# Kernel optimization log

Measured on AMD Instinct MI355X. Metric: run time of the kernel, lower is better.

The kernel has to match this reference:

```python
import jax, jax.numpy as jnp
import numpy as np

D_MODEL = 768
N_HEADS = 12
HEAD = D_MODEL // N_HEADS  # 64


def setup_inputs() -> dict:
    key = jax.random.key(0)
    ks = jax.random.split(key, 9)
    s = 1.0 / np.sqrt(D_MODEL)
    x = jax.random.normal(ks[0], (2, 2048, D_MODEL), dtype=jnp.float32)
    # per-head Q/K/V projection weights stacked over heads: [H, d_model, head]
    Wq = jax.random.uniform(ks[1], (N_HEADS, D_MODEL, HEAD), minval=-s, maxval=s, dtype=jnp.float32)
    Wk = jax.random.uniform(ks[2], (N_HEADS, D_MODEL, HEAD), minval=-s, maxval=s, dtype=jnp.float32)
    Wv = jax.random.uniform(ks[3], (N_HEADS, D_MODEL, HEAD), minval=-s, maxval=s, dtype=jnp.float32)
    bq = jax.random.uniform(ks[4], (N_HEADS, HEAD), minval=-s, maxval=s, dtype=jnp.float32)
    bk = jax.random.uniform(ks[5], (N_HEADS, HEAD), minval=-s, maxval=s, dtype=jnp.float32)
    bv = jax.random.uniform(ks[6], (N_HEADS, HEAD), minval=-s, maxval=s, dtype=jnp.float32)
    Wo = jax.random.uniform(ks[7], (D_MODEL, D_MODEL), minval=-s, maxval=s, dtype=jnp.float32)
    bo = jax.random.uniform(ks[8], (D_MODEL,), minval=-s, maxval=s, dtype=jnp.float32)
    return {"x": x, "Wq": Wq, "Wk": Wk, "Wv": Wv, "bq": bq, "bk": bk, "bv": bv, "Wo": Wo, "bo": bo}


def reference(x, Wq, Wk, Wv, bq, bk, bv, Wo, bo):
    # x: [B, S, D]; weights stacked over heads [H, D, hd]
    Q = jnp.einsum('bsd,hde->bhse', x, Wq) + bq[None, :, None, :]
    K = jnp.einsum('bsd,hde->bhse', x, Wk) + bk[None, :, None, :]
    V = jnp.einsum('bsd,hde->bhse', x, Wv) + bv[None, :, None, :]
    scores = jnp.einsum('bhse,bhte->bhst', Q, K) / jnp.sqrt(jnp.float32(HEAD))
    attn = jax.nn.softmax(scores, axis=-1)  # [B, H, S, S]
    out = jnp.einsum('bhst,bhte->bhse', attn, V)  # [B, H, S, hd]
    B, H, S, E = out.shape
    out = out.transpose(0, 2, 1, 3).reshape(B, S, H * E)  # concat heads -> [B, S, D]
    return out @ Wo + bo
```

## Files before the change

### kernel.cpp

```cpp
#include <hip/hip_runtime.h>
#include <hip/hip_bf16.h>

typedef __bf16 bf16x8 __attribute__((ext_vector_type(8)));
typedef __bf16 bf16x4 __attribute__((ext_vector_type(4)));
typedef float  f32x4  __attribute__((ext_vector_type(4)));
typedef short  short4v __attribute__((ext_vector_type(4)));

#define MFMA_16x16x32(a,b,c) __builtin_amdgcn_mfma_f32_16x16x32_bf16((a),(b),(c),0,0,0)

#if __has_builtin(__builtin_amdgcn_mfma_f32_16x16x16_bf16)
__device__ inline f32x4 MFMA16(bf16x4 a, bf16x4 b, f32x4 c){
  return __builtin_amdgcn_mfma_f32_16x16x16_bf16(a, b, c, 0, 0, 0);
}
#elif __has_builtin(__builtin_amdgcn_mfma_f32_16x16x16bf16_1k)
__device__ inline f32x4 MFMA16(bf16x4 a, bf16x4 b, f32x4 c){
  return __builtin_amdgcn_mfma_f32_16x16x16bf16_1k(
      __builtin_bit_cast(short4v, a), __builtin_bit_cast(short4v, b), c, 0, 0, 0);
}
#else
__device__ inline f32x4 MFMA16(bf16x4 a, bf16x4 b, f32x4 c){
  f32x4 d;
  asm volatile("v_mfma_f32_16x16x16_bf16 %0, %1, %2, %3"
               : "=v"(d) : "v"(a), "v"(b), "v"(c));
  return d;
}
#endif

#if __has_builtin(__builtin_amdgcn_exp2f)
#define EXP2(x) __builtin_amdgcn_exp2f(x)
#else
extern "C" __device__ float __ocml_native_exp2_f32(float);
#define EXP2(x) __ocml_native_exp2_f32(x)
#endif

#if __has_builtin(__builtin_amdgcn_global_load_lds)
#define HAS_GLDS 1
__device__ inline void glds16(const __bf16* g, __bf16* l){
  __builtin_amdgcn_global_load_lds(
      (const __attribute__((address_space(1))) unsigned int*)g,
      (__attribute__((address_space(3))) unsigned int*)l, 16, 0, 0);
}
#else
#define HAS_GLDS 0
#endif

static constexpr int DM = 768;
static constexpr int NH = 12;
static constexpr int HD = 64;
static constexpr int BB = 2;
static constexpr int SS = 2048;
static constexpr int NR = BB*SS;
static constexpr int NC = 3*DM;
static constexpr int RTOT = BB*NH*SS;
static constexpr float SCALEQ = 0.125f * 1.4426950408889634f;

__device__ inline int xcd_swz(int b, int n){
  return (n % 8 == 0) ? (b % 8) * (n >> 3) + (b >> 3) : b;
}

static constexpr int PB_X = NR*DM/(4*256);
static constexpr int PB_W = 3*12*12;
static constexpr int PB_O = 12*12;
static constexpr int PB_B = (NC+255)/256;
__global__ __launch_bounds__(256) void k_prep(const float* __restrict__ x,
    const float* __restrict__ Wq, const float* __restrict__ Wk,
    const float* __restrict__ Wv, const float* __restrict__ bq,
    const float* __restrict__ bk, const float* __restrict__ bv,
    const float* __restrict__ Wo,
    __bf16* __restrict__ xb, __bf16* __restrict__ Wt,
    __bf16* __restrict__ WoT, float* __restrict__ bqkv)
{
  __shared__ float tile[64][65];
  const int blk = blockIdx.x, tid = threadIdx.x;
  if (blk < PB_X){
    int i = blk*256 + tid;
    float4 v = reinterpret_cast<const float4*>(x)[i];
    bf16x4 o; o[0]=(__bf16)v.x; o[1]=(__bf16)v.y; o[2]=(__bf16)v.z; o[3]=(__bf16)v.w;
    reinterpret_cast<bf16x4*>(xb)[i] = o;
  } else if (blk < PB_X + PB_W){
    int b2 = blk - PB_X;
    int dt = b2 % 12, h = (b2/12) % 12, m = b2/144;
    const float* W = (m==0)?Wq:((m==1)?Wk:Wv);
    float scale = (m==0)?SCALEQ:1.0f;
    int tx = tid & 63, ty = tid >> 6;
    #pragma unroll
    for (int i=0;i<16;i++){
      int dl = ty*16+i;
      tile[dl][tx] = W[(h*DM + dt*64 + dl)*HD + tx];
    }
    __syncthreads();
    #pragma unroll
    for (int i=0;i<16;i++){
      int e = ty*16+i;
      Wt[(size_t)(m*DM + h*HD + e)*DM + dt*64 + tx] = (__bf16)(tile[tx][e]*scale);
    }
  } else if (blk < PB_X + PB_W + PB_O){
    int b2 = blk - PB_X - PB_W;
    int dt = b2 % 12, ct = b2/12;
    int tx = tid & 63, ty = tid >> 6;
    #pragma unroll
    for (int i=0;i<16;i++){
      int dl = ty*16+i;
      tile[dl][tx] = Wo[(dt*64+dl)*DM + ct*64 + tx];
    }
    __syncthreads();
    #pragma unroll
    for (int i=0;i<16;i++){
      int cl = ty*16+i;
      WoT[(size_t)(ct*64+cl)*DM + dt*64 + tx] = (__bf16)tile[tx][cl];
    }
  } else {
    int c = (blk - PB_X - PB_W - PB_O)*256 + tid;
    if (c < NC){
      int m = c/DM, r = c - m*DM;
      const float* s = (m==0)?bq:((m==1)?bk:bv);
      bqkv[c] = s[r] * ((m==0)?SCALEQ:1.0f);
    }
  }
}

template<int BM, int EPI>
__global__ __launch_bounds__(256) void k_gemm(
    const __bf16* __restrict__ A, const __bf16* __restrict__ Bt,
    const float* __restrict__ bias, float* __restrict__ outF,
    __bf16* __restrict__ qb, __bf16* __restrict__ kb, __bf16* __restrict__ vb,
    int M, int N)
{
  constexpr int BN = 128, BK = 64;
  constexpr int K = DM;
  constexpr int HM = BM/2;
  constexpr int MR = BM/32;
  __shared__ __align__(16) __bf16 As[BM][BK];
  __shared__ __align__(16) __bf16 Bs[BN][BK];
  const int tid = threadIdx.x;
  const int w = tid>>6, lane = tid&63, g = lane>>4, r15 = lane&15;
  const int wr = w>>1, wc = w&1;
  const int nTM = M/BM;
  const int bx = xcd_swz(blockIdx.x, gridDim.x);
  const int mt = bx % nTM, nt = bx / nTM;
  const int m0 = mt*BM, n0 = nt*BN;

  const int rrel = lane>>3, seg = lane&7;
  const int ssrc = seg ^ rrel;

  f32x4 acc[MR][4];
  #pragma unroll
  for (int i=0;i<MR;i++)
    #pragma unroll
    for (int j=0;j<4;j++) acc[i][j] = f32x4{0.f,0.f,0.f,0.f};

  for (int k0=0;k0<K;k0+=BK){
#if HAS_GLDS
    #pragma unroll
    for (int c=0;c<BM/32;c++)
      glds16(&A[(size_t)(m0 + w*(BM/4) + c*8 + rrel)*K + k0 + ssrc*8],
             &As[w*(BM/4) + c*8][0]);
    #pragma unroll
    for (int c=0;c<4;c++)
      glds16(&Bt[(size_t)(n0 + w*32 + c*8 + rrel)*K + k0 + ssrc*8],
             &Bs[w*32 + c*8][0]);
#else
    #pragma unroll
    for (int c=0;c<BM/32;c++)
      *reinterpret_cast<uint4*>(&As[w*(BM/4) + c*8 + rrel][seg*8]) =
        *reinterpret_cast<const uint4*>(&A[(size_t)(m0 + w*(BM/4) + c*8 + rrel)*K + k0 + ssrc*8]);
    #pragma unroll
    for (int c=0;c<4;c++)
      *reinterpret_cast<uint4*>(&Bs[w*32 + c*8 + rrel][seg*8]) =
        *reinterpret_cast<const uint4*>(&Bt[(size_t)(n0 + w*32 + c*8 + rrel)*K + k0 + ssrc*8]);
#endif
    __syncthreads();
    bf16x8 af[MR][2], bfr[4][2];
    #pragma unroll
    for (int mi=0;mi<MR;mi++){
      int row = wr*HM + mi*16 + r15;
      #pragma unroll
      for (int c2=0;c2<2;c2++)
        af[mi][c2] = *reinterpret_cast<const bf16x8*>(&As[row][8*((c2*4+g) ^ (row&7))]);
    }
    #pragma unroll
    for (int ni=0;ni<4;ni++){
      int row = wc*64 + ni*16 + r15;
      #pragma unroll
      for (int c2=0;c2<2;c2++)
        bfr[ni][c2] = *reinterpret_cast<const bf16x8*>(&Bs[row][8*((c2*4+g) ^ (row&7))]);
    }
    #pragma unroll
    for (int c2=0;c2<2;c2++)
      #pragma unroll
      for (int mi=0;mi<MR;mi++)
        #pragma unroll
        for (int ni=0;ni<4;ni++)
          acc[mi][ni] = MFMA_16x16x32(af[mi][c2], bfr[ni][c2], acc[mi][ni]);
    __syncthreads();
  }

  #pragma unroll
  for (int mi=0;mi<MR;mi++){
    #pragma unroll
    for (int ni=0;ni<4;ni++){
      int row0 = m0 + wr*HM + mi*16 + 4*g;
      int col  = n0 + wc*64 + ni*16 + r15;
      float bc = bias[col];
      #pragma unroll
      for (int r=0;r<4;r++){
        float val = acc[mi][ni][r] + bc;
        int rr = row0 + r;
        if (EPI==1){
          outF[(size_t)rr*DM + col] = val;
        } else {
          int b = rr >> 11, s = rr & 2047;
          int m = col >= 2*DM ? 2 : (col >= DM ? 1 : 0);
          int c2 = col - m*DM, hh = c2>>6, ee = c2&63;
          __bf16* dst = (m==0) ? qb : ((m==1) ? kb : vb);
          dst[(((size_t)b*NH + hh)*SS + s)*HD + ee] = (__bf16)val;
        }
      }
    }
  }
}

__global__ __launch_bounds__(256) void k_vt(const __bf16* __restrict__ Vr,
                                            __bf16* __restrict__ Vt){
  __shared__ __align__(16) __bf16 tile[64][72];
  const int tid = threadIdx.x;
  const int bh = blockIdx.x >> 5, tt = blockIdx.x & 31;
  const int t0 = tt*64;
  const __bf16* src = Vr + (size_t)bh*SS*HD;
  __bf16* dst = Vt + (size_t)bh*HD*SS;
  const int rt = tid>>3, seg = tid&7;
  #pragma unroll
  for (int p=0;p<2;p++){
    int t = t0 + rt + 32*p;
    bf16x8 v = *reinterpret_cast<const bf16x8*>(&src[(size_t)t*HD + seg*8]);
    #pragma unroll
    for (int j=0;j<8;j++) tile[seg*8+j][rt+32*p - t0 + t0] = v[j];
  }
  __syncthreads();
  #pragma unroll
  for (int p=0;p<2;p++){
    int e = rt + 32*p;
    *reinterpret_cast<uint4*>(&dst[(size_t)e*SS + t0 + seg*8]) =
      *reinterpret_cast<const uint4*>(&tile[e][seg*8]);
  }
}

__global__ __launch_bounds__(256) void k_attn(
    const __bf16* __restrict__ Qb, const __bf16* __restrict__ Kb,
    const __bf16* __restrict__ Vt, float* __restrict__ oP,
    float* __restrict__ lP, __bf16* __restrict__ AO, int kvLen)
{
  constexpr int TT = 64, SK = 72;
  __shared__ __align__(16) __bf16 Ks[TT][SK];
  __shared__ __align__(16) __bf16 Vs[HD][SK];
  const int tid = threadIdx.x, w = tid>>6, lane = tid&63, g = lane>>4, r15 = lane&15;
  const int bx = xcd_swz(blockIdx.x, gridDim.x);
  const int qt = bx & 15, bh = bx >> 4;
  const int q0 = qt*128 + w*32;
  const int kv0 = blockIdx.y * kvLen;
  const __bf16* Qh = Qb + (size_t)bh*SS*HD;
  const __bf16* Kh = Kb + (size_t)bh*SS*HD;
  const __bf16* Vh = Vt + (size_t)bh*HD*SS;

  bf16x8 qf[2][2];
  #pragma unroll
  for (int sub=0; sub<2; sub++){
    int qrow = q0 + sub*16 + r15;
    qf[sub][0] = *reinterpret_cast<const bf16x8*>(&Qh[qrow*HD + g*8]);
    qf[sub][1] = *reinterpret_cast<const bf16x8*>(&Qh[qrow*HD + 32 + g*8]);
  }

  f32x4 o[2][4];
  #pragma unroll
  for (int s2=0;s2<2;s2++)
    #pragma unroll
    for (int i=0;i<4;i++) o[s2][i] = f32x4{0.f,0.f,0.f,0.f};
  f32x4 ol[2] = {f32x4{0.f,0.f,0.f,0.f}, f32x4{0.f,0.f,0.f,0.f}};
  const bf16x4 vones = {(__bf16)1.0f, (__bf16)1.0f, (__bf16)1.0f, (__bf16)1.0f};

  const int row0 = tid>>3,        seg0 = tid&7;
  const int row1 = (tid+256)>>3,  seg1 = tid&7;
  const int vcol0 = 32*(seg0>>2) + 16*(seg0&1) + 4*((seg0>>1)&1);

  {
    uint4 k0v = *reinterpret_cast<const uint4*>(&Kh[(kv0+row0)*HD + seg0*8]);
    uint4 k1v = *reinterpret_cast<const uint4*>(&Kh[(kv0+row1)*HD + seg1*8]);
    uint4 v0v = *reinterpret_cast<const uint4*>(&Vh[(size_t)row0*SS + kv0 + seg0*8]);
    uint4 v1v = *reinterpret_cast<const uint4*>(&Vh[(size_t)row1*SS + kv0 + seg1*8]);
    *reinterpret_cast<uint4*>(&Ks[row0][seg0*8]) = k0v;
    *reinterpret_cast<uint4*>(&Ks[row1][seg1*8]) = k1v;
    *reinterpret_cast<uint2*>(&Vs[row0][vcol0])     = uint2{v0v.x, v0v.y};
    *reinterpret_cast<uint2*>(&Vs[row0][vcol0 + 8]) = uint2{v0v.z, v0v.w};
    *reinterpret_cast<uint2*>(&Vs[row1][vcol0])     = uint2{v1v.x, v1v.y};
    *reinterpret_cast<uint2*>(&Vs[row1][vcol0 + 8]) = uint2{v1v.z, v1v.w};
  }
  __syncthreads();

  for (int t0 = kv0; t0 < kv0 + kvLen; t0 += TT){
    const bool hasNext = (t0 + TT) < kv0 + kvLen;
    uint4 k0v, k1v, v0v, v1v;
    if (hasNext){
      k0v = *reinterpret_cast<const uint4*>(&Kh[(t0+TT+row0)*HD + seg0*8]);
      k1v = *reinterpret_cast<const uint4*>(&Kh[(t0+TT+row1)*HD + seg1*8]);
      v0v = *reinterpret_cast<const uint4*>(&Vh[(size_t)row0*SS + t0+TT + seg0*8]);
      v1v = *reinterpret_cast<const uint4*>(&Vh[(size_t)row1*SS + t0+TT + seg1*8]);
    }

    bf16x8 kf0[4], kf1[4];
    #pragma unroll
    for (int jt=0;jt<4;jt++){
      kf0[jt] = *reinterpret_cast<const bf16x8*>(&Ks[jt*16 + r15][g*8]);
      kf1[jt] = *reinterpret_cast<const bf16x8*>(&Ks[jt*16 + r15][32 + g*8]);
    }
    bf16x8 vf[4][2];
    #pragma unroll
    for (int et=0;et<4;et++)
      #pragma unroll
      for (int p=0;p<2;p++)
        vf[et][p] = *reinterpret_cast<const bf16x8*>(&Vs[et*16 + r15][p*32 + g*8]);

    __syncthreads();

    if (hasNext){
      *reinterpret_cast<uint4*>(&Ks[row0][seg0*8]) = k0v;
      *reinterpret_cast<uint4*>(&Ks[row1][seg1*8]) = k1v;
      *reinterpret_cast<uint2*>(&Vs[row0][vcol0])     = uint2{v0v.x, v0v.y};
      *reinterpret_cast<uint2*>(&Vs[row0][vcol0 + 8]) = uint2{v0v.z, v0v.w};
      *reinterpret_cast<uint2*>(&Vs[row1][vcol0])     = uint2{v1v.x, v1v.y};
      *reinterpret_cast<uint2*>(&Vs[row1][vcol0 + 8]) = uint2{v1v.z, v1v.w};
    }

    f32x4 sc[2][4];
    __builtin_amdgcn_s_setprio(1);
    #pragma unroll
    for (int sub=0; sub<2; sub++)
      #pragma unroll
      for (int jt=0;jt<4;jt++){
        f32x4 t = f32x4{0.f,0.f,0.f,0.f};
        t = MFMA_16x16x32(kf0[jt], qf[sub][0], t);
        t = MFMA_16x16x32(kf1[jt], qf[sub][1], t);
        sc[sub][jt] = t;
      }
    __builtin_amdgcn_s_setprio(0);

    bf16x4 pa[2][4];
    #pragma unroll
    for (int sub=0; sub<2; sub++)
      #pragma unroll
      for (int ks=0;ks<4;ks++){
        pa[sub][ks][0] = (__bf16)EXP2(sc[sub][ks][0]);
        pa[sub][ks][1] = (__bf16)EXP2(sc[sub][ks][1]);
        pa[sub][ks][2] = (__bf16)EXP2(sc[sub][ks][2]);
        pa[sub][ks][3] = (__bf16)EXP2(sc[sub][ks][3]);
      }

    __builtin_amdgcn_s_setprio(1);
    #pragma unroll
    for (int sub=0; sub<2; sub++){
      #pragma unroll
      for (int et=0;et<4;et++)
        #pragma unroll
        for (int ks=0;ks<4;ks++){
          bf16x8 vv = vf[et][ks>>1];
          bf16x4 vq = (ks & 1) ? bf16x4{vv[4],vv[5],vv[6],vv[7]}
                               : bf16x4{vv[0],vv[1],vv[2],vv[3]};
          o[sub][et] = MFMA16(pa[sub][ks], vq, o[sub][et]);
        }
      #pragma unroll
      for (int ks=0;ks<4;ks++)
        ol[sub] = MFMA16(pa[sub][ks], vones, ol[sub]);
    }
    __builtin_amdgcn_s_setprio(0);

    __syncthreads();
  }

  const bool direct = (gridDim.y == 1);
  const int b = bh/NH, h = bh - b*NH;
  const size_t pbase = (size_t)blockIdx.y * RTOT + bh*SS;
  #pragma unroll
  for (int sub=0; sub<2; sub++){
    if (direct){
      #pragma unroll
      for (int r=0;r<4;r++){
        float linv = 1.0f / ol[sub][r];
        int s = q0 + sub*16 + 4*g + r;
        #pragma unroll
        for (int et=0;et<4;et++)
          AO[((size_t)(b*SS + s))*DM + h*HD + et*16 + r15] = (__bf16)(o[sub][et][r]*linv);
      }
    } else {
      if (r15 == 0){
        #pragma unroll
        for (int r=0;r<4;r++)
          lP[pbase + q0 + sub*16 + 4*g + r] = ol[sub][r];
      }
      #pragma unroll
      for (int r=0;r<4;r++){
        size_t rid = pbase + q0 + sub*16 + 4*g + r;
        #pragma unroll
        for (int et=0;et<4;et++)
          oP[rid*HD + et*16 + r15] = o[sub][et][r];
      }
    }
  }
}

__global__ __launch_bounds__(256) void k_merge(
    const float* __restrict__ oP, const float* __restrict__ lP,
    __bf16* __restrict__ AO, int nsplit)
{
  int t = blockIdx.x*256 + threadIdx.x;
  int rid = t >> 4, e0 = (t & 15)*4;
  int bh = rid >> 11, s = rid & 2047;
  int b = bh/NH, h = bh - b*NH;

  float lsum = 0.f;
  float acc[4] = {0.f,0.f,0.f,0.f};
  for (int sp=0; sp<nsplit; sp++){
    lsum += lP[(size_t)sp*RTOT + rid];
    float4 v = *reinterpret_cast<const float4*>(&oP[((size_t)sp*RTOT + rid)*HD + e0]);
    acc[0] += v.x; acc[1] += v.y; acc[2] += v.z; acc[3] += v.w;
  }
  float inv = 1.0f/lsum;
  size_t base = ((size_t)(b*SS + s))*DM + h*HD + e0;
  #pragma unroll
  for (int j=0;j<4;j++) AO[base + j] = (__bf16)(acc[j]*inv);
}

extern "C" void kernel_launch(void* const* d_in, const int* in_sizes, int n_in,
                              void* d_out, int out_size, void* d_ws, size_t ws_size,
                              hipStream_t stream) {
  const float* x  = (const float*)d_in[0];
  const float* Wq = (const float*)d_in[1];
  const float* Wk = (const float*)d_in[2];
  const float* Wv = (const float*)d_in[3];
  const float* bq = (const float*)d_in[4];
  const float* bk = (const float*)d_in[5];
  const float* bv = (const float*)d_in[6];
  const float* Wo = (const float*)d_in[7];
  const float* bo = (const float*)d_in[8];
  float* out = (float*)d_out;

  char* ws = (char*)d_ws;
  size_t off = 0;
  auto alloc = [&](size_t bytes) -> void* {
    void* p = ws + off;
    off += (bytes + 255) & ~size_t(255);
    return p;
  };
  __bf16* xb   = (__bf16*)alloc((size_t)NR*DM*2);
  __bf16* wt   = (__bf16*)alloc((size_t)NC*DM*2);
  float*  bqkv = (float*) alloc((size_t)NC*4);
  __bf16* wot  = (__bf16*)alloc((size_t)DM*DM*2);
  __bf16* qb2  = (__bf16*)alloc((size_t)BB*NH*SS*HD*2);
  __bf16* kb2  = (__bf16*)alloc((size_t)BB*NH*SS*HD*2);
  __bf16* vb2  = (__bf16*)alloc((size_t)BB*NH*SS*HD*2);
  __bf16* vt2  = (__bf16*)alloc((size_t)BB*NH*SS*HD*2);
  __bf16* aob  = (__bf16*)alloc((size_t)NR*DM*2);
  float*  lP   = (float*) alloc((size_t)2*RTOT*4);
  size_t  oP_off = off;
  float*  oP   = (float*)(ws + oP_off);
  auto fits = [&](int ns){ return oP_off + (size_t)ns*RTOT*HD*4 <= ws_size; };
  const int nsplit = fits(2) ? 2 : 1;

  k_prep<<<PB_X + PB_W + PB_O + PB_B, 256, 0, stream>>>(
      x, Wq, Wk, Wv, bq, bk, bv, Wo, xb, wt, wot, bqkv);

  k_gemm<128,0><<<(NR/128)*(NC/128), 256, 0, stream>>>(
      xb, wt, bqkv, nullptr, qb2, kb2, vb2, NR, NC);

  k_vt<<<BB*NH*(SS/64), 256, 0, stream>>>(vb2, vt2);

  dim3 agrid(BB*NH*(SS/128), nsplit);
  k_attn<<<agrid, 256, 0, stream>>>(qb2, kb2, vt2, oP, lP, aob, SS/nsplit);
  if (nsplit > 1)
    k_merge<<<(RTOT*16)/256, 256, 0, stream>>>(oP, lP, aob, nsplit);

  k_gemm<64,1><<<(NR/64)*(DM/128), 256, 0, stream>>>(
      aob, wot, bo, out, nullptr, nullptr, nullptr, NR, DM);
}
```

Measured before the change: 119.0 us.

## Double-buffer K/V shared tiles and compute softmax row sums in registers

Shared K/V tiles become double-buffered, so the next tile is written into the alternate buffer after the MFMAs and one barrier per iteration is removed. The row-sum accumulation moves off the MFMA unit: instead of multiplying probabilities by a ones vector, each lane sums its fp32 exponentials, and the partial sums are reduced with cross-lane shuffles at the end. This cuts MFMA issue count and synchronisation at the cost of doubled LDS usage, which may lower occupancy, plus a few extra VALU adds. The sums now use unrounded fp32 values rather than bf16, which changes numerics slightly.

```diff
diff --git a/kernel.cpp b/kernel.cpp
--- a/kernel.cpp
+++ b/kernel.cpp
@@ -234,7 +234,7 @@
     int t = t0 + rt + 32*p;
     bf16x8 v = *reinterpret_cast<const bf16x8*>(&src[(size_t)t*HD + seg*8]);
     #pragma unroll
-    for (int j=0;j<8;j++) tile[seg*8+j][rt+32*p - t0 + t0] = v[j];
+    for (int j=0;j<8;j++) tile[seg*8+j][rt+32*p] = v[j];
   }
   __syncthreads();
   #pragma unroll
@@ -251,8 +251,8 @@
     float* __restrict__ lP, __bf16* __restrict__ AO, int kvLen)
 {
   constexpr int TT = 64, SK = 72;
-  __shared__ __align__(16) __bf16 Ks[TT][SK];
-  __shared__ __align__(16) __bf16 Vs[HD][SK];
+  __shared__ __align__(16) __bf16 Ks[2][TT][SK];
+  __shared__ __align__(16) __bf16 Vs[2][HD][SK];
   const int tid = threadIdx.x, w = tid>>6, lane = tid&63, g = lane>>4, r15 = lane&15;
   const int bx = xcd_swz(blockIdx.x, gridDim.x);
   const int qt = bx & 15, bh = bx >> 4;
@@ -275,8 +275,7 @@
   for (int s2=0;s2<2;s2++)
     #pragma unroll
     for (int i=0;i<4;i++) o[s2][i] = f32x4{0.f,0.f,0.f,0.f};
-  f32x4 ol[2] = {f32x4{0.f,0.f,0.f,0.f}, f32x4{0.f,0.f,0.f,0.f}};
-  const bf16x4 vones = {(__bf16)1.0f, (__bf16)1.0f, (__bf16)1.0f, (__bf16)1.0f};
+  float psum[2] = {0.f, 0.f};
 
   const int row0 = tid>>3,        seg0 = tid&7;
   const int row1 = (tid+256)>>3,  seg1 = tid&7;
@@ -287,15 +286,16 @@
     uint4 k1v = *reinterpret_cast<const uint4*>(&Kh[(kv0+row1)*HD + seg1*8]);
     uint4 v0v = *reinterpret_cast<const uint4*>(&Vh[(size_t)row0*SS + kv0 + seg0*8]);
     uint4 v1v = *reinterpret_cast<const uint4*>(&Vh[(size_t)row1*SS + kv0 + seg1*8]);
-    *reinterpret_cast<uint4*>(&Ks[row0][seg0*8]) = k0v;
-    *reinterpret_cast<uint4*>(&Ks[row1][seg1*8]) = k1v;
-    *reinterpret_cast<uint2*>(&Vs[row0][vcol0])     = uint2{v0v.x, v0v.y};
-    *reinterpret_cast<uint2*>(&Vs[row0][vcol0 + 8]) = uint2{v0v.z, v0v.w};
-    *reinterpret_cast<uint2*>(&Vs[row1][vcol0])     = uint2{v1v.x, v1v.y};
-    *reinterpret_cast<uint2*>(&Vs[row1][vcol0 + 8]) = uint2{v1v.z, v1v.w};
+    *reinterpret_cast<uint4*>(&Ks[0][row0][seg0*8]) = k0v;
+    *reinterpret_cast<uint4*>(&Ks[0][row1][seg1*8]) = k1v;
+    *reinterpret_cast<uint2*>(&Vs[0][row0][vcol0])     = uint2{v0v.x, v0v.y};
+    *reinterpret_cast<uint2*>(&Vs[0][row0][vcol0 + 8]) = uint2{v0v.z, v0v.w};
+    *reinterpret_cast<uint2*>(&Vs[0][row1][vcol0])     = uint2{v1v.x, v1v.y};
+    *reinterpret_cast<uint2*>(&Vs[0][row1][vcol0 + 8]) = uint2{v1v.z, v1v.w};
   }
   __syncthreads();
 
+  int cur = 0;
   for (int t0 = kv0; t0 < kv0 + kvLen; t0 += TT){
     const bool hasNext = (t0 + TT) < kv0 + kvLen;
     uint4 k0v, k1v, v0v, v1v;
@@ -309,26 +309,15 @@
     bf16x8 kf0[4], kf1[4];
     #pragma unroll
     for (int jt=0;jt<4;jt++){
-      kf0[jt] = *reinterpret_cast<const bf16x8*>(&Ks[jt*16 + r15][g*8]);
-      kf1[jt] = *reinterpret_cast<const bf16x8*>(&Ks[jt*16 + r15][32 + g*8]);
+      kf0[jt] = *reinterpret_cast<const bf16x8*>(&Ks[cur][jt*16 + r15][g*8]);
+      kf1[jt] = *reinterpret_cast<const bf16x8*>(&Ks[cur][jt*16 + r15][32 + g*8]);
     }
     bf16x8 vf[4][2];
     #pragma unroll
     for (int et=0;et<4;et++)
       #pragma unroll
       for (int p=0;p<2;p++)
-        vf[et][p] = *reinterpret_cast<const bf16x8*>(&Vs[et*16 + r15][p*32 + g*8]);
-
-    __syncthreads();
-
-    if (hasNext){
-      *reinterpret_cast<uint4*>(&Ks[row0][seg0*8]) = k0v;
-      *reinterpret_cast<uint4*>(&Ks[row1][seg1*8]) = k1v;
-      *reinterpret_cast<uint2*>(&Vs[row0][vcol0])     = uint2{v0v.x, v0v.y};
-      *reinterpret_cast<uint2*>(&Vs[row0][vcol0 + 8]) = uint2{v0v.z, v0v.w};
-      *reinterpret_cast<uint2*>(&Vs[row1][vcol0])     = uint2{v1v.x, v1v.y};
-      *reinterpret_cast<uint2*>(&Vs[row1][vcol0 + 8]) = uint2{v1v.z, v1v.w};
-    }
+        vf[et][p] = *reinterpret_cast<const bf16x8*>(&Vs[cur][et*16 + r15][p*32 + g*8]);
 
     f32x4 sc[2][4];
     __builtin_amdgcn_s_setprio(1);
@@ -348,15 +337,18 @@
     for (int sub=0; sub<2; sub++)
       #pragma unroll
       for (int ks=0;ks<4;ks++){
-        pa[sub][ks][0] = (__bf16)EXP2(sc[sub][ks][0]);
-        pa[sub][ks][1] = (__bf16)EXP2(sc[sub][ks][1]);
-        pa[sub][ks][2] = (__bf16)EXP2(sc[sub][ks][2]);
-        pa[sub][ks][3] = (__bf16)EXP2(sc[sub][ks][3]);
+        float p0 = EXP2(sc[sub][ks][0]);
+        float p1 = EXP2(sc[sub][ks][1]);
+        float p2 = EXP2(sc[sub][ks][2]);
+        float p3 = EXP2(sc[sub][ks][3]);
+        pa[sub][ks][0] = (__bf16)p0; pa[sub][ks][1] = (__bf16)p1;
+        pa[sub][ks][2] = (__bf16)p2; pa[sub][ks][3] = (__bf16)p3;
+        psum[sub] += (p0 + p1) + (p2 + p3);
       }
 
     __builtin_amdgcn_s_setprio(1);
     #pragma unroll
-    for (int sub=0; sub<2; sub++){
+    for (int sub=0; sub<2; sub++)
       #pragma unroll
       for (int et=0;et<4;et++)
         #pragma unroll
@@ -366,13 +358,19 @@
                                : bf16x4{vv[0],vv[1],vv[2],vv[3]};
           o[sub][et] = MFMA16(pa[sub][ks], vq, o[sub][et]);
         }
-      #pragma unroll
-      for (int ks=0;ks<4;ks++)
-        ol[sub] = MFMA16(pa[sub][ks], vones, ol[sub]);
-    }
     __builtin_amdgcn_s_setprio(0);
 
+    if (hasNext){
+      int nxt = cur ^ 1;
+      *reinterpret_cast<uint4*>(&Ks[nxt][row0][seg0*8]) = k0v;
+      *reinterpret_cast<uint4*>(&Ks[nxt][row1][seg1*8]) = k1v;
+      *reinterpret_cast<uint2*>(&Vs[nxt][row0][vcol0])     = uint2{v0v.x, v0v.y};
+      *reinterpret_cast<uint2*>(&Vs[nxt][row0][vcol0 + 8]) = uint2{v0v.z, v0v.w};
+      *reinterpret_cast<uint2*>(&Vs[nxt][row1][vcol0])     = uint2{v1v.x, v1v.y};
+      *reinterpret_cast<uint2*>(&Vs[nxt][row1][vcol0 + 8]) = uint2{v1v.z, v1v.w};
+    }
     __syncthreads();
+    cur ^= 1;
   }
 
   const bool direct = (gridDim.y == 1);
@@ -380,21 +378,24 @@
   const size_t pbase = (size_t)blockIdx.y * RTOT + bh*SS;
   #pragma unroll
   for (int sub=0; sub<2; sub++){
+    float lv = psum[sub];
+    lv += __shfl_xor(lv, 16);
+    lv += __shfl_xor(lv, 32);
     if (direct){
+      float linv = 1.0f / lv;
+      float li[4];
+      #pragma unroll
+      for (int r=0;r<4;r++) li[r] = __shfl(linv, 4*g + r);
       #pragma unroll
       for (int r=0;r<4;r++){
-        float linv = 1.0f / ol[sub][r];
         int s = q0 + sub*16 + 4*g + r;
         #pragma unroll
         for (int et=0;et<4;et++)
-          AO[((size_t)(b*SS + s))*DM + h*HD + et*16 + r15] = (__bf16)(o[sub][et][r]*linv);
+          AO[((size_t)(b*SS + s))*DM + h*HD + et*16 + r15] = (__bf16)(o[sub][et][r]*li[r]);
       }
     } else {
-      if (r15 == 0){
-        #pragma unroll
-        for (int r=0;r<4;r++)
-          lP[pbase + q0 + sub*16 + 4*g + r] = ol[sub][r];
-      }
+      if (g == 0)
+        lP[pbase + q0 + sub*16 + r15] = lv;
       #pragma unroll
       for (int r=0;r<4;r++){
         size_t rid = pbase + q0 + sub*16 + 4*g + r;
```

New measurement: 118.5 us. About the same (-0.4%).
